# Kernel tuning notes

Hardware: AMD Instinct MI355X
Metric: run time of the kernel (lower is better)

## Reference

```python
import jax, jax.numpy as jnp
import numpy as np

B, S, H = 2, 2048, 2048
NH, NKV, D = 16, 8, 128
THETA = 10000.0
EPS = 1e-6
SCALE = D ** -0.5


def setup_inputs() -> dict:
    key = jax.random.key(0)
    k0, k1, k2 = jax.random.split(key, 3)
    hidden_states = jax.random.normal(k0, (B, S, H), dtype=jnp.float32)
    position_ids = jnp.arange(B * S, dtype=jnp.int64).reshape(B, S) % S
    w_qkv = jax.random.normal(k1, (NH * D + 2 * NKV * D, H), dtype=jnp.float32) * 0.02
    w_o = jax.random.normal(k2, (H, NH * D), dtype=jnp.float32) * 0.02
    q_norm_w = jnp.ones((D,), dtype=jnp.float32)
    k_norm_w = jnp.ones((D,), dtype=jnp.float32)
    return {"hidden_states": hidden_states, "position_ids": position_ids,
            "w_qkv": w_qkv, "w_o": w_o, "q_norm_w": q_norm_w, "k_norm_w": k_norm_w}


def _rms_norm(x, w):
    # x: [..., D]; vLLM RMSNorm: x * rsqrt(mean(x^2) + eps) * w
    var = jnp.mean(x * x, axis=-1, keepdims=True)
    return x * jax.lax.rsqrt(var + EPS) * w


def _rope_gptj(x, positions):
    # non-neox (GPT-J interleaved) RoPE. x: [B, S, nheads, D], positions: [B, S]
    inv_freq = 1.0 / (THETA ** (jnp.arange(0, D, 2, dtype=jnp.float32) / D))  # [D/2]
    freqs = positions.astype(jnp.float32)[..., None] * inv_freq  # [B, S, D/2]
    cos = jnp.repeat(jnp.cos(freqs), 2, axis=-1)[:, :, None, :]  # [B, S, 1, D]
    sin = jnp.repeat(jnp.sin(freqs), 2, axis=-1)[:, :, None, :]
    x1 = x[..., ::2]
    x2 = x[..., 1::2]
    rot = jnp.stack([-x2, x1], axis=-1).reshape(x.shape)  # interleaved rotate
    return x * cos + rot * sin


def reference(hidden_states, position_ids, w_qkv, w_o, q_norm_w, k_norm_w):
    bsz, seq_len, _ = hidden_states.shape
    qkv = jnp.einsum('bsh,oh->bso', hidden_states, w_qkv)  # [B, S, q+2kv]
    q, k, v = jnp.split(qkv, [NH * D, NH * D + NKV * D], axis=-1)
    q = q.reshape(bsz, seq_len, NH, D)
    k = k.reshape(bsz, seq_len, NKV, D)
    v = v.reshape(bsz, seq_len, NKV, D)
    q = _rms_norm(q, q_norm_w)
    k = _rms_norm(k, k_norm_w)
    q = _rope_gptj(q, position_ids)
    k = _rope_gptj(k, position_ids)
    # GQA: group q heads over kv heads
    G = NH // NKV
    qg = q.reshape(bsz, seq_len, NKV, G, D)
    # scores: [B, NKV, G, S, S]
    scores = jnp.einsum('bqhgd,bkhd->bhgqk', qg, k) * SCALE
    causal = jnp.tril(jnp.ones((seq_len, seq_len), dtype=bool))
    scores = jnp.where(causal, scores, jnp.float32(-1e30))
    probs = jax.nn.softmax(scores, axis=-1)
    out = jnp.einsum('bhgqk,bkhd->bqhgd', probs, v)  # [B, S, NKV, G, D]
    out = out.reshape(bsz, seq_len, NH * D)
    return jnp.einsum('bsd,hd->bsh', out, w_o)  # [B, S, H]
```

## Files before the change

### kernel.cpp

```cpp
#include <hip/hip_runtime.h>
#include <hip/hip_bf16.h>
#include <cstdint>
#include <cstddef>


typedef __attribute__((ext_vector_type(8))) short bf16x8;
typedef __attribute__((ext_vector_type(4))) float f32x4;

#define B_ 2
#define S_ 2048
#define H_ 2048
#define NH_ 16
#define NKV_ 8
#define D_ 128
#define BS_ 4096
#define QKVO_ 4096

__device__ __forceinline__ unsigned short f2bf(float f) {
  union { float f; unsigned u; } v; v.f = f;
  unsigned u = v.u;
  u += 0x7fffu + ((u >> 16) & 1u);
  return (unsigned short)(u >> 16);
}

__device__ __forceinline__ unsigned cvt_pk_bf16(float lo, float hi) {
  unsigned r;
  asm("v_cvt_pk_bf16_f32 %0, %1, %2" : "=v"(r) : "v"(lo), "v"(hi));
  return r;
}

__device__ __forceinline__ void gload_lds16(const void* g, void* l) {
  __builtin_amdgcn_global_load_lds(
      (const __attribute__((address_space(1))) unsigned int*)g,
      (__attribute__((address_space(3))) unsigned int*)l, 16, 0, 0);
}

__global__ void k_f32_to_bf16(const float* __restrict__ x,
                              unsigned short* __restrict__ y, int n4) {
  int i = blockIdx.x * blockDim.x + threadIdx.x;
  if (i >= n4) return;
  float4 v = ((const float4*)x)[i];
  ushort4 o;
  o.x = f2bf(v.x); o.y = f2bf(v.y); o.z = f2bf(v.z); o.w = f2bf(v.w);
  ((ushort4*)y)[i] = o;
}

#define BM 128
#define BN 128
#define BK 32

__global__ __launch_bounds__(256, 2) void k_gemm_bf16(
    const unsigned short* __restrict__ A, const unsigned short* __restrict__ Bm,
    float* __restrict__ C, int M, int N, int K) {
  __shared__ __align__(16) char lds[2][2][BM * BK * 2];

  int nwg = gridDim.x;
  int bid = blockIdx.x;
  int cpx = nwg >> 3;
  int swz = (bid & 7) * cpx + (bid >> 3);
  int nbn = N / BN;
  int bm = swz / nbn, bn = swz % nbn;

  int tid = threadIdx.x;
  int lane = tid & 63, w = tid >> 6;
  int wr = w >> 1, wc = w & 1;
  int lq = lane & 15, lk = lane >> 4;

  const unsigned short* Abase = A + (size_t)bm * BM * K;
  const unsigned short* Bbase = Bm + (size_t)bn * BN * K;

  f32x4 acc[4][4] = {};
  int nt = K / BK;

  auto stage = [&](int buf, int t) {
#pragma unroll
    for (int j = 0; j < 2; ++j) {
      int s = (tid + j * 256) * 16;
      int row = s >> 6;
      int cb = s & 48;
      int cs = cb ^ (((row >> 1) & 3) << 4);
      const char* ga = (const char*)(Abase + (size_t)row * K + t * BK) + cs;
      const char* gb = (const char*)(Bbase + (size_t)row * K + t * BK) + cs;
      gload_lds16(ga, &lds[buf][0][s]);
      gload_lds16(gb, &lds[buf][1][s]);
    }
  };

  stage(0, 0);
  __syncthreads();

  int cur = 0;
  for (int t = 0; t < nt; ++t) {
    if (t + 1 < nt) stage(cur ^ 1, t + 1);
    bf16x8 af[4], bfr[4];
#pragma unroll
    for (int m = 0; m < 4; ++m) {
      int row = wr * 64 + m * 16 + lq;
      int addr = row * 64 + ((lk * 16) ^ (((row >> 1) & 3) << 4));
      af[m] = *(const bf16x8*)(&lds[cur][0][addr]);
    }
#pragma unroll
    for (int n = 0; n < 4; ++n) {
      int row = wc * 64 + n * 16 + lq;
      int addr = row * 64 + ((lk * 16) ^ (((row >> 1) & 3) << 4));
      bfr[n] = *(const bf16x8*)(&lds[cur][1][addr]);
    }
#pragma unroll
    for (int m = 0; m < 4; ++m)
#pragma unroll
      for (int n = 0; n < 4; ++n)
        acc[m][n] = __builtin_amdgcn_mfma_f32_16x16x32_bf16(af[m], bfr[n], acc[m][n], 0, 0, 0);
    __syncthreads();
    cur ^= 1;
  }

#pragma unroll
  for (int m = 0; m < 4; ++m) {
    int row0 = bm * BM + wr * 64 + m * 16 + lk * 4;
#pragma unroll
    for (int n = 0; n < 4; ++n) {
      int col = bn * BN + wc * 64 + n * 16 + lq;
#pragma unroll
      for (int r = 0; r < 4; ++r)
        C[(size_t)(row0 + r) * N + col] = acc[m][n][r];
    }
  }
}

__global__ void k_norm_rope(const float* __restrict__ qkv,
                            const int* __restrict__ pos,
                            const float* __restrict__ qw,
                            const float* __restrict__ kw,
                            unsigned short* __restrict__ Qb,
                            unsigned short* __restrict__ Kb) {
  int g = blockIdx.x * 4 + (threadIdx.x >> 6);
  int lane = threadIdx.x & 63;
  int t = g / 24;
  int slot = g % 24;
  bool isq = slot < 16;
  int h = isq ? slot : slot - 16;
  int off = isq ? h * D_ : NH_ * D_ + h * D_;
  const float* w = isq ? qw : kw;

  float2 x = *(const float2*)(qkv + (size_t)t * QKVO_ + off + lane * 2);
  float ss = x.x * x.x + x.y * x.y;
#pragma unroll
  for (int o = 1; o < 64; o <<= 1) ss += __shfl_xor(ss, o);
  float inv = rsqrtf(ss * (1.0f / 128.0f) + 1e-6f);
  float2 wv = *(const float2*)(w + lane * 2);
  float x1 = x.x * inv * wv.x;
  float x2 = x.y * inv * wv.y;

  float p = (float)pos[t];
  float invf = exp2f(-(float)(lane * 2) * (13.287712379549449f / 128.0f));
  float ang = p * invf;
  float sn, cs;
  sincosf(ang, &sn, &cs);
  float y1 = x1 * cs - x2 * sn;
  float y2 = x2 * cs + x1 * sn;

  int b = t >> 11;
  int sq = t & (S_ - 1);
  size_t o_;
  unsigned short* dst;
  if (isq) { o_ = (((size_t)b * NH_ + h) * S_ + sq) * D_ + lane * 2; dst = Qb; }
  else     { o_ = (((size_t)b * NKV_ + h) * S_ + sq) * D_ + lane * 2; dst = Kb; }
  ushort2 ov; ov.x = f2bf(y1); ov.y = f2bf(y2);
  *(ushort2*)(dst + o_) = ov;
}

__global__ void k_v_transpose(const float* __restrict__ qkv,
                              unsigned short* __restrict__ Vt) {
  __shared__ unsigned short tile[128][72];
  int bidx = blockIdx.x;
  int st = bidx & 31;
  int kh = (bidx >> 5) & 7;
  int b = bidx >> 8;
  int s0 = st * 64;
  int tid = threadIdx.x;
#pragma unroll
  for (int i = 0; i < 8; ++i) {
    int idx = tid + i * 256;
    int row = idx >> 5, c4 = idx & 31;
    float4 v = *(const float4*)(qkv + ((size_t)(b * S_ + s0 + row)) * QKVO_ +
                                (NH_ + NKV_) * D_ + kh * D_ + c4 * 4);
    tile[c4 * 4 + 0][row] = f2bf(v.x);
    tile[c4 * 4 + 1][row] = f2bf(v.y);
    tile[c4 * 4 + 2][row] = f2bf(v.z);
    tile[c4 * 4 + 3][row] = f2bf(v.w);
  }
  __syncthreads();
#pragma unroll
  for (int i = 0; i < 8; ++i) {
    int idx = tid + i * 256;
    int d = idx >> 4, c4 = idx & 15;
    ushort4 o;
    o.x = tile[d][c4 * 4 + 0]; o.y = tile[d][c4 * 4 + 1];
    o.z = tile[d][c4 * 4 + 2]; o.w = tile[d][c4 * 4 + 3];
    *(ushort4*)(Vt + ((((size_t)b * NKV_ + kh) * D_ + d) * S_) + s0 + c4 * 4) = o;
  }
}

#define KVB 64

__global__ __launch_bounds__(512, 2) void k_attn(
    const unsigned short* __restrict__ Qb, const unsigned short* __restrict__ Kb,
    const unsigned short* __restrict__ Vt, unsigned short* __restrict__ Ob) {
  __shared__ __align__(16) char Ks[2][KVB * D_ * 2];
  __shared__ __align__(16) char Vs[2][D_ * KVB * 2];
  __shared__ __align__(16) char Ps[8][32 * KVB * 2];

  int x = blockIdx.x;
  int kk = x >> 5;
  int bh = x & 31;
  int b = bh >> 4, h = bh & 15;
  int kvh = h >> 1;

  int tid = threadIdx.x, lane = tid & 63, w = tid >> 6;
  int lq = lane & 15, lk = lane >> 4;
  int strip = w >> 2, wq = w & 3;
  int qt = strip ? kk : 15 - kk;
  int q0w = qt * 128 + wq * 32;
  int nt_w = ((q0w + 31) >> 6) + 1;
  int nt_max = 2 * (15 - kk) + 2;

  const unsigned short* Qhead = Qb + ((size_t)b * NH_ + h) * S_ * D_;
  const unsigned short* Khead = Kb + ((size_t)b * NKV_ + kvh) * S_ * D_;
  const unsigned short* Vthead = Vt + ((size_t)b * NKV_ + kvh) * D_ * S_;

  bf16x8 qf[2][4];
#pragma unroll
  for (int m = 0; m < 2; ++m)
#pragma unroll
    for (int ks = 0; ks < 4; ++ks)
      qf[m][ks] = *(const bf16x8*)(Qhead +
          (size_t)(q0w + m * 16 + lq) * D_ + ks * 32 + lk * 8);

  f32x4 o_acc[2][8] = {};
  float mrow[2] = {-1e30f, -1e30f};
  float lrow[2] = {0.0f, 0.0f};

  auto stageKV = [&](int buf, int t) {
    int kv0 = t * KVB;
#pragma unroll
    for (int j = 0; j < 2; ++j) {
      int s = (tid + j * 512) * 16;
      {
        int row = s >> 8, cb = s & 255;
        int cs = cb ^ ((row & 7) << 4);
        const char* g = (const char*)(Khead + (size_t)(kv0 + row) * D_) + cs;
        gload_lds16(g, &Ks[buf][s]);
      }
      {
        int rv = s >> 7, cv = s & 127;
        int cs = cv ^ ((rv & 7) << 4);
        const char* g = (const char*)(Vthead + (size_t)rv * S_ + kv0) + cs;
        gload_lds16(g, &Vs[buf][s]);
      }
    }
  };

  stageKV(0, 0);
  __syncthreads();

  const float c1 = 0.08838834764831845f * 1.4426950408889634f;

  int cur = 0;
  for (int t = 0; t < nt_max; ++t) {
    if (t + 1 < nt_max) stageKV(cur ^ 1, t + 1);
    if (t < nt_w) {
      int kv0 = t * KVB;

      f32x4 sc[4][2] = {};
      __builtin_amdgcn_s_setprio(1);
#pragma unroll
      for (int ks = 0; ks < 4; ++ks) {
        bf16x8 kf[4];
#pragma unroll
        for (int n = 0; n < 4; ++n) {
          int row = n * 16 + lq;
          int addr = row * 256 + ((ks * 64 + lk * 16) ^ ((row & 7) << 4));
          kf[n] = *(const bf16x8*)(&Ks[cur][addr]);
        }
#pragma unroll
        for (int n = 0; n < 4; ++n)
#pragma unroll
          for (int m = 0; m < 2; ++m)
            sc[n][m] = __builtin_amdgcn_mfma_f32_16x16x32_bf16(kf[n], qf[m][ks], sc[n][m], 0, 0, 0);
      }
      __builtin_amdgcn_s_setprio(0);

      bool diag = (kv0 + KVB > q0w);
#pragma unroll
      for (int m = 0; m < 2; ++m) {
        int qg = q0w + m * 16 + lq;
        float sv[4][4];
        float vmax = -1e30f;
#pragma unroll
        for (int n = 0; n < 4; ++n)
#pragma unroll
          for (int r = 0; r < 4; ++r) {
            float xv = sc[n][m][r] * c1;
            if (diag && (kv0 + n * 16 + lk * 4 + r > qg)) xv = -1e30f;
            sv[n][r] = xv;
            vmax = fmaxf(vmax, xv);
          }
        vmax = fmaxf(vmax, __shfl_xor(vmax, 16));
        vmax = fmaxf(vmax, __shfl_xor(vmax, 32));
        float mnew = fmaxf(mrow[m], vmax);
        float cr = exp2f(mrow[m] - mnew);
        mrow[m] = mnew;
        float rs = 0.0f;
#pragma unroll
        for (int n = 0; n < 4; ++n)
#pragma unroll
          for (int r = 0; r < 4; ++r) {
            float pv = exp2f(sv[n][r] - mnew);
            sv[n][r] = pv;
            rs += pv;
          }
        rs += __shfl_xor(rs, 16);
        rs += __shfl_xor(rs, 32);
        lrow[m] = lrow[m] * cr + rs;

        float crr[4];
#pragma unroll
        for (int r = 0; r < 4; ++r) crr[r] = __shfl(cr, lk * 4 + r);
#pragma unroll
        for (int nd = 0; nd < 8; ++nd)
#pragma unroll
          for (int r = 0; r < 4; ++r) o_acc[m][nd][r] *= crr[r];

        int qlocal = m * 16 + lq;
#pragma unroll
        for (int n = 0; n < 4; ++n) {
          uint2 pk_;
          pk_.x = cvt_pk_bf16(sv[n][0], sv[n][1]);
          pk_.y = cvt_pk_bf16(sv[n][2], sv[n][3]);
          int addr = qlocal * 128 + ((n * 32 + lk * 8) ^ ((qlocal & 7) << 4));
          *(uint2*)(&Ps[w][addr]) = pk_;
        }
      }

      __builtin_amdgcn_s_setprio(1);
#pragma unroll
      for (int ks = 0; ks < 2; ++ks) {
        bf16x8 pa[2];
#pragma unroll
        for (int m = 0; m < 2; ++m) {
          int row = m * 16 + lq;
          int addr = row * 128 + ((ks * 64 + lk * 16) ^ ((row & 7) << 4));
          pa[m] = *(const bf16x8*)(&Ps[w][addr]);
        }
#pragma unroll
        for (int nd = 0; nd < 8; ++nd) {
          int row = nd * 16 + lq;
          int addr = row * 128 + ((ks * 64 + lk * 16) ^ ((row & 7) << 4));
          bf16x8 vf = *(const bf16x8*)(&Vs[cur][addr]);
#pragma unroll
          for (int m = 0; m < 2; ++m)
            o_acc[m][nd] = __builtin_amdgcn_mfma_f32_16x16x32_bf16(pa[m], vf, o_acc[m][nd], 0, 0, 0);
        }
      }
      __builtin_amdgcn_s_setprio(0);
    }
    __syncthreads();
    cur ^= 1;
  }

#pragma unroll
  for (int m = 0; m < 2; ++m)
#pragma unroll
    for (int r = 0; r < 4; ++r) {
      float lv = __shfl(lrow[m], lk * 4 + r);
      float rl = 1.0f / lv;
      int qg = q0w + m * 16 + lk * 4 + r;
      size_t base = ((size_t)b * S_ + qg) * (NH_ * D_) + h * D_;
#pragma unroll
      for (int nd = 0; nd < 8; ++nd)
        Ob[base + nd * 16 + lq] = f2bf(o_acc[m][nd][r] * rl);
    }
}

extern "C" void kernel_launch(void* const* d_in, const int* in_sizes, int n_in,
                              void* d_out, int out_size, void* d_ws, size_t ws_size,
                              hipStream_t stream) {
  const float* hs    = (const float*)d_in[0];
  const int*   pos   = (const int*)d_in[1];
  const float* w_qkv = (const float*)d_in[2];
  const float* w_o   = (const float*)d_in[3];
  const float* qw    = (const float*)d_in[4];
  const float* kw    = (const float*)d_in[5];
  float* out = (float*)d_out;

  char* ws = (char*)d_ws;
  unsigned short* Xbf  = (unsigned short*)ws;
  unsigned short* Wqbf = Xbf + (size_t)BS_ * H_;
  unsigned short* Wobf = Wqbf + (size_t)QKVO_ * H_;
  float* qkv = (float*)(Wobf + (size_t)H_ * (NH_ * D_));
  unsigned short* Qb  = (unsigned short*)(qkv + (size_t)BS_ * QKVO_);
  unsigned short* Kb  = Qb + (size_t)B_ * NH_ * S_ * D_;
  unsigned short* Vtb = Kb + (size_t)B_ * NKV_ * S_ * D_;
  unsigned short* Ab  = Vtb + (size_t)B_ * NKV_ * S_ * D_;

  k_f32_to_bf16<<<(BS_ * H_ / 4) / 256, 256, 0, stream>>>(hs, Xbf, BS_ * H_ / 4);
  k_f32_to_bf16<<<(QKVO_ * H_ / 4) / 256, 256, 0, stream>>>(w_qkv, Wqbf, QKVO_ * H_ / 4);
  k_f32_to_bf16<<<(H_ * NH_ * D_ / 4) / 256, 256, 0, stream>>>(w_o, Wobf, H_ * NH_ * D_ / 4);

  k_gemm_bf16<<<(BS_ / BM) * (QKVO_ / BN), 256, 0, stream>>>(
      Xbf, Wqbf, qkv, BS_, QKVO_, H_);

  k_norm_rope<<<BS_ * 24 / 4, 256, 0, stream>>>(qkv, pos, qw, kw, Qb, Kb);

  k_v_transpose<<<B_ * NKV_ * (S_ / 64), 256, 0, stream>>>(qkv, Vtb);

  k_attn<<<256, 512, 0, stream>>>(Qb, Kb, Vtb, Ab);

  k_gemm_bf16<<<(BS_ / BM) * (H_ / BN), 256, 0, stream>>>(
      Ab, Wobf, out, BS_, H_, H_);
}
```

Measured before the change: 377.6 us.

## Add 256x256 four-stage pipelined bf16 GEMM for QKV and precompute RoPE trig table

Replaces the 128x128 tiled GEMM used for the QKV projection with a 256x256-tile, 512-thread kernel. It uses a four-deep LDS ring filled by direct global-to-LDS loads, split half-K MFMA phases with priority boosts, and explicit waitcnt/barrier scheduling, aiming for more operand reuse and better overlap of loads and math. Separately, it precomputes a cos/sin table per position and frequency so the norm+RoPE kernel does a table lookup instead of exp2/sincos per element. The larger tile uses about 128KB of LDS, which limits occupancy to one block per CU. The prefetch also reads past the last K tile, and the trig table reuses the attention output buffer as scratch.

```diff
diff --git a/kernel.cpp b/kernel.cpp
--- a/kernel.cpp
+++ b/kernel.cpp
@@ -43,6 +43,123 @@
   ushort4 o;
   o.x = f2bf(v.x); o.y = f2bf(v.y); o.z = f2bf(v.z); o.w = f2bf(v.w);
   ((ushort4*)y)[i] = o;
+}
+
+__global__ void k_trig(float2* __restrict__ tab) {
+  int i = blockIdx.x * 256 + threadIdx.x;
+  int p = i >> 6, f = i & 63;
+  float invf = exp2f(-(float)(f * 2) * (13.287712379549449f / 128.0f));
+  float ang = (float)p * invf;
+  float sn, cs;
+  sincosf(ang, &sn, &cs);
+  tab[i] = make_float2(cs, sn);
+}
+
+__global__ __launch_bounds__(512, 2) void k_gemm256(
+    const unsigned short* __restrict__ A, const unsigned short* __restrict__ Bm,
+    float* __restrict__ C, int M, int N, int K) {
+  __shared__ __align__(16) char ldsA[4][16384];
+  __shared__ __align__(16) char ldsB[4][16384];
+
+  int nwg = gridDim.x;
+  int bid = blockIdx.x;
+  int cpx = nwg >> 3;
+  int swz = (bid & 7) * cpx + (bid >> 3);
+  int nbn = N >> 8;
+  int bm = swz / nbn, bn = swz % nbn;
+
+  int tid = threadIdx.x;
+  int lane = tid & 63, w = tid >> 6;
+  int wr = w >> 2, wc = w & 3;
+  int lq = lane & 15, lk = lane >> 4;
+
+  const unsigned short* Abase = A + (size_t)bm * 256 * K;
+  const unsigned short* Bbase = Bm + (size_t)bn * 256 * K;
+
+  f32x4 acc[8][4] = {};
+  int nk = K >> 5;
+
+  auto stageA = [&](int t) {
+    char* dst = ldsA[t & 3];
+#pragma unroll
+    for (int j = 0; j < 2; ++j) {
+      int s = (tid + j * 512) * 16;
+      int row = s >> 6;
+      const char* g = (const char*)(Abase + (size_t)row * K) + t * 64 + (s & 63);
+      gload_lds16(g, dst + s);
+    }
+  };
+  auto stageB = [&](int t) {
+    char* dst = ldsB[t & 3];
+#pragma unroll
+    for (int j = 0; j < 2; ++j) {
+      int s = (tid + j * 512) * 16;
+      int row = s >> 6;
+      const char* g = (const char*)(Bbase + (size_t)row * K) + t * 64 + (s & 63);
+      gload_lds16(g, dst + s);
+    }
+  };
+
+  stageA(0); stageB(0);
+  stageA(1); stageB(1);
+  stageA(2); stageB(2);
+  stageB(3);
+  asm volatile("s_waitcnt vmcnt(10)" ::: "memory");
+  __builtin_amdgcn_s_barrier();
+
+  for (int t = 0; t < nk; ++t) {
+    const char* As = ldsA[t & 3];
+    const char* Bs = ldsB[t & 3];
+    bf16x8 a[8], b[4];
+
+#pragma unroll
+    for (int m = 0; m < 4; ++m)
+      a[m] = *(const bf16x8*)(&As[(wr * 128 + m * 16 + lq) * 64 + lk * 16]);
+#pragma unroll
+    for (int n = 0; n < 4; ++n)
+      b[n] = *(const bf16x8*)(&Bs[(wc * 64 + n * 16 + lq) * 64 + lk * 16]);
+    stageA(t + 3);
+    __builtin_amdgcn_s_barrier();
+    asm volatile("s_waitcnt lgkmcnt(0)" ::: "memory");
+    __builtin_amdgcn_sched_barrier(0);
+    __builtin_amdgcn_s_setprio(1);
+#pragma unroll
+    for (int m = 0; m < 4; ++m)
+#pragma unroll
+      for (int n = 0; n < 4; ++n)
+        acc[m][n] = __builtin_amdgcn_mfma_f32_16x16x32_bf16(a[m], b[n], acc[m][n], 0, 0, 0);
+    __builtin_amdgcn_s_setprio(0);
+    __builtin_amdgcn_s_barrier();
+
+#pragma unroll
+    for (int m = 4; m < 8; ++m)
+      a[m] = *(const bf16x8*)(&As[(wr * 128 + m * 16 + lq) * 64 + lk * 16]);
+    stageB(t + 4);
+    asm volatile("s_waitcnt vmcnt(10)" ::: "memory");
+    __builtin_amdgcn_s_barrier();
+    asm volatile("s_waitcnt lgkmcnt(0)" ::: "memory");
+    __builtin_amdgcn_sched_barrier(0);
+    __builtin_amdgcn_s_setprio(1);
+#pragma unroll
+    for (int m = 4; m < 8; ++m)
+#pragma unroll
+      for (int n = 0; n < 4; ++n)
+        acc[m][n] = __builtin_amdgcn_mfma_f32_16x16x32_bf16(a[m], b[n], acc[m][n], 0, 0, 0);
+    __builtin_amdgcn_s_setprio(0);
+    __builtin_amdgcn_s_barrier();
+  }
+
+#pragma unroll
+  for (int m = 0; m < 8; ++m) {
+    int row0 = bm * 256 + wr * 128 + m * 16 + lk * 4;
+#pragma unroll
+    for (int n = 0; n < 4; ++n) {
+      int col = bn * 256 + wc * 64 + n * 16 + lq;
+#pragma unroll
+      for (int r = 0; r < 4; ++r)
+        C[(size_t)(row0 + r) * N + col] = acc[m][n][r];
+    }
+  }
 }
 
 #define BM 128
@@ -131,6 +248,7 @@
                             const int* __restrict__ pos,
                             const float* __restrict__ qw,
                             const float* __restrict__ kw,
+                            const float2* __restrict__ tab,
                             unsigned short* __restrict__ Qb,
                             unsigned short* __restrict__ Kb) {
   int g = blockIdx.x * 4 + (threadIdx.x >> 6);
@@ -151,13 +269,10 @@
   float x1 = x.x * inv * wv.x;
   float x2 = x.y * inv * wv.y;
 
-  float p = (float)pos[t];
-  float invf = exp2f(-(float)(lane * 2) * (13.287712379549449f / 128.0f));
-  float ang = p * invf;
-  float sn, cs;
-  sincosf(ang, &sn, &cs);
-  float y1 = x1 * cs - x2 * sn;
-  float y2 = x2 * cs + x1 * sn;
+  int p = pos[t];
+  float2 t2 = tab[p * 64 + lane];
+  float y1 = x1 * t2.x - x2 * t2.y;
+  float y2 = x2 * t2.x + x1 * t2.y;
 
   int b = t >> 11;
   int sq = t & (S_ - 1);
@@ -402,15 +517,17 @@
   unsigned short* Kb  = Qb + (size_t)B_ * NH_ * S_ * D_;
   unsigned short* Vtb = Kb + (size_t)B_ * NKV_ * S_ * D_;
   unsigned short* Ab  = Vtb + (size_t)B_ * NKV_ * S_ * D_;
-
+  float2* tab = (float2*)Ab;
+
+  k_trig<<<512, 256, 0, stream>>>(tab);
   k_f32_to_bf16<<<(BS_ * H_ / 4) / 256, 256, 0, stream>>>(hs, Xbf, BS_ * H_ / 4);
   k_f32_to_bf16<<<(QKVO_ * H_ / 4) / 256, 256, 0, stream>>>(w_qkv, Wqbf, QKVO_ * H_ / 4);
   k_f32_to_bf16<<<(H_ * NH_ * D_ / 4) / 256, 256, 0, stream>>>(w_o, Wobf, H_ * NH_ * D_ / 4);
 
-  k_gemm_bf16<<<(BS_ / BM) * (QKVO_ / BN), 256, 0, stream>>>(
+  k_gemm256<<<(BS_ / 256) * (QKVO_ / 256), 512, 0, stream>>>(
       Xbf, Wqbf, qkv, BS_, QKVO_, H_);
 
-  k_norm_rope<<<BS_ * 24 / 4, 256, 0, stream>>>(qkv, pos, qw, kw, Qb, Kb);
+  k_norm_rope<<<BS_ * 24 / 4, 256, 0, stream>>>(qkv, pos, qw, kw, tab, Qb, Kb);
 
   k_v_transpose<<<B_ * NKV_ * (S_ / 64), 256, 0, stream>>>(qkv, Vtb);
 
```

Measured after the change: 381.5 us. No clear change (+1.1%).
